# Kernel optimization log

Hardware: AMD Instinct MI355X
Metric: run time of the kernel (lower is better)

The kernel has to match this reference:

```python
import jax, jax.numpy as jnp
import numpy as np

N_NODES = 50000
N_EDGES = 600000
N_GRAPHS = 512
DIM = 128
N_FEAT = 78
N_LAYERS = 4
BN_EPS = 1e-5


def setup_inputs() -> dict:
    key = jax.random.key(0)
    ks = jax.random.split(key, 12)
    w = lambda k, s: (jax.random.normal(k, s, jnp.float32) * 0.05)
    x = jax.random.normal(ks[0], (N_NODES, N_FEAT), jnp.float32)
    edge_index = jax.random.randint(ks[1], (2, N_EDGES), 0, N_NODES)
    batch = jnp.sort(jax.random.randint(ks[2], (N_NODES,), 0, N_GRAPHS))
    return {
        "x": x,
        "edge_index": edge_index,
        "batch": batch,
        "ini_w1": w(ks[3], (N_FEAT, DIM)),
        "ini_b1": jnp.zeros((DIM,), jnp.float32),
        "ini_w2": w(ks[4], (DIM, DIM)),
        "ini_b2": jnp.zeros((DIM,), jnp.float32),
        "gin_w1": w(ks[5], (N_LAYERS, DIM, DIM)),
        "gin_b1": jnp.zeros((N_LAYERS, DIM), jnp.float32),
        "gin_w2": w(ks[6], (N_LAYERS, DIM, DIM)),
        "gin_b2": jnp.zeros((N_LAYERS, DIM), jnp.float32),
        "bn_gamma": jnp.ones((N_LAYERS, DIM), jnp.float32),
        "bn_beta": jnp.zeros((N_LAYERS, DIM), jnp.float32),
        "layer_w": w(ks[7], (N_LAYERS,)),  # Conv2d(L,1,(1,1)) weight
        "layer_b": jnp.zeros((1,), jnp.float32),
    }


def reference(x, edge_index, batch, ini_w1, ini_b1, ini_w2, ini_b2,
              gin_w1, gin_b1, gin_w2, gin_b2, bn_gamma, bn_beta,
              layer_w, layer_b):
    # ini_embed: Linear -> ReLU -> Linear
    h = jnp.maximum(x @ ini_w1 + ini_b1, 0.0) @ ini_w2 + ini_b2  # [N, D]
    src, dst = edge_index[0], edge_index[1]
    embeds = []
    for i in range(N_LAYERS):
        # GINConv (eps=0): mlp(x_i + sum_{j->i} x_j)
        agg = jax.ops.segment_sum(h[src], dst, num_segments=N_NODES)
        z = h + agg
        z = jnp.maximum(z @ gin_w1[i] + gin_b1[i], 0.0) @ gin_w2[i] + gin_b2[i]
        z = jnp.maximum(z, 0.0)  # F.relu after conv
        # BatchNorm1d (training mode: batch stats, biased var)
        mean = jnp.mean(z, axis=0)
        var = jnp.mean((z - mean) ** 2, axis=0)
        h = (z - mean) * jax.lax.rsqrt(var + BN_EPS) * bn_gamma[i] + bn_beta[i]
        embeds.append(h)
    layer_nodes = jnp.stack(embeds, axis=1)  # [N, L, D]
    # layer_conv Conv2d(L,1,(1,1)): learned weighted sum over layer axis + bias
    pos_global_node = jnp.einsum('nld,l->nd', layer_nodes, layer_w) + layer_b
    # global_add_pool over graphs
    pos_global_graph = jax.ops.segment_sum(pos_global_node, batch,
                                           num_segments=N_GRAPHS)  # [G, D]
    return pos_global_graph
```

## Files before the change

kernel.cpp:

```cpp
#include <hip/hip_runtime.h>

#define N_NODES  50000
#define N_EDGES  600000
#define N_GRAPHS 512
#define DIM      128
#define N_FEAT   78
#define N_LAYERS 4
#define BN_EPS   1e-5f
#define SLOT_CAP 64
#define LDA      136
#define NPART    16

#define NBKT     196
#define NBLK_BIN 128
#define BCAP     64
#define EDGES_PER_BIN ((N_EDGES + NBLK_BIN - 1) / NBLK_BIN)

#define GSTART_BLOCKS 196
#define ZERO_BLOCKS 512
#define GBLOCKS ((N_NODES + 63) / 64)
#define TW_ELEMS (10 * 16384)
#define BN_FLOATS (N_LAYERS * NPART * 256)
#define TWB ((TW_ELEMS + BN_FLOATS + 255) / 256)

typedef __attribute__((ext_vector_type(8))) _Float16 f16x8;
typedef __attribute__((ext_vector_type(4))) float f32x4;

static __device__ __forceinline__ short f2h(float f) {
    _Float16 h = (_Float16)f;
    union { _Float16 h; short s; } u; u.h = h;
    return u.s;
}
static __device__ __forceinline__ float h2f(ushort s) {
    union { ushort s; _Float16 h; } u; u.s = s;
    return (float)u.h;
}


__global__ __launch_bounds__(256) void prep(const float* __restrict__ ini_w1,
                                            const float* __restrict__ ini_w2,
                                            const float* __restrict__ gw1,
                                            const float* __restrict__ gw2,
                                            short* __restrict__ wt,
                                            float* __restrict__ bnstat,
                                            const int* __restrict__ src,
                                            const int* __restrict__ dst,
                                            const int* __restrict__ batch,
                                            int* __restrict__ bcnt,
                                            uint* __restrict__ bpool,
                                            int* __restrict__ gstart,
                                            float* __restrict__ gsum,
                                            float* __restrict__ gssq) {
    __shared__ int lcur[NBKT];
    int tid = threadIdx.x;
    int b = blockIdx.x;
    if (b < TWB) {
        int gid = b * 256 + tid;
        if (gid < TW_ELEMS) {
            int m = gid >> 14;
            int idx = gid & 16383;
            int n = idx >> 7;
            int k = idx & 127;
            const float* s;
            int K = 128;
            if (m == 0) { s = ini_w1; K = N_FEAT; }
            else if (m == 1) s = ini_w2;
            else if (m < 6) s = gw1 + (m - 2) * 16384;
            else s = gw2 + (m - 6) * 16384;
            float v = (k < K) ? s[k * 128 + n] : 0.f;
            wt[m * 16384 + n * 128 + k] = f2h(v);
        } else {
            int bi = gid - TW_ELEMS;
            if (bi < BN_FLOATS) bnstat[bi] = 0.0f;
        }
        return;
    }
    b -= TWB;
    if (b < NBLK_BIN) {
        for (int i = tid; i < NBKT; i += 256) lcur[i] = 0;
        __syncthreads();
        int base = b * EDGES_PER_BIN;
        int lim = min(base + EDGES_PER_BIN, N_EDGES);
        for (int e = base + tid; e < lim; e += 256) {
            int d = dst[e];
            int s = src[e];
            int bk = d >> 8;
            int p = atomicAdd(&lcur[bk], 1);
            if (p < BCAP)
                bpool[(bk * NBLK_BIN + b) * BCAP + p] =
                    ((uint)(d & 255) << 16) | (uint)s;
        }
        __syncthreads();
        for (int i = tid; i < NBKT; i += 256) bcnt[b * NBKT + i] = lcur[i];
        return;
    }
    b -= NBLK_BIN;
    if (b < GSTART_BLOCKS) {
        int n = b * 256 + tid;
        if (n < N_NODES) {
            int g = batch[n];
            int gp = (n == 0) ? -1 : batch[n - 1];
            for (int gg = gp + 1; gg <= g; ++gg) gstart[gg] = n;
            if (n == N_NODES - 1)
                for (int gg = g + 1; gg <= N_GRAPHS; ++gg) gstart[gg] = N_NODES;
        }
        return;
    }
    b -= GSTART_BLOCKS;
    float4 z = make_float4(0.f, 0.f, 0.f, 0.f);
    float* bse = (b < 256) ? gsum : gssq;
    int off = (b & 255) * 1024 + tid * 4;
    *(float4*)&bse[off] = z;
}


__global__ __launch_bounds__(256, 4) void ini_fused(const float* __restrict__ x,
                                                    const short* __restrict__ Wt1,
                                                    const float* __restrict__ b1,
                                                    const short* __restrict__ Wt2,
                                                    const float* __restrict__ b2,
                                                    ushort* __restrict__ Cout,
                                                    const uint* __restrict__ bpool,
                                                    const int* __restrict__ bcnt,
                                                    int* __restrict__ cnt,
                                                    ushort* __restrict__ slot) {
    __shared__ short smem[2 * 64 * LDA];
    int tid = threadIdx.x;

    if (blockIdx.x >= GBLOCKS) {
        int bkt = blockIdx.x - GBLOCKS;
        ushort* lslot = (ushort*)smem;
        int* lcnt = (int*)((char*)smem + 32768);
        int* rcnt = (int*)((char*)smem + 33792);
        lcnt[tid] = 0;
        if (tid < NBLK_BIN) rcnt[tid] = min(bcnt[tid * NBKT + bkt], BCAP);
        __syncthreads();
        const uint* pool = bpool + (size_t)bkt * NBLK_BIN * BCAP;
        #pragma unroll 1
        for (int i = tid; i < NBLK_BIN * BCAP; i += 256) {
            int run = i >> 6;
            int pos = i & (BCAP - 1);
            if (pos < rcnt[run]) {
                uint u = pool[i];
                int ls = u >> 16;
                int p = atomicAdd(&lcnt[ls], 1);
                if (p < SLOT_CAP) lslot[ls * SLOT_CAP + p] = (ushort)(u & 0xffffu);
            }
        }
        __syncthreads();
        {
            int n2 = min(lcnt[tid], SLOT_CAP);
            ushort* L = lslot + tid * SLOT_CAP;
            for (int i = 1; i < n2; ++i) {
                ushort key = L[i];
                int j = i - 1;
                while (j >= 0 && L[j] > key) { L[j + 1] = L[j]; --j; }
                L[j + 1] = key;
            }
        }
        __syncthreads();
        int node0 = bkt << 8;
        int gn = node0 + tid;
        if (gn < N_NODES) cnt[gn] = lcnt[tid];
        #pragma unroll
        for (int j = 0; j < 8; ++j) {
            int i = tid + j * 256;
            int r = i >> 3;
            int c = i & 7;
            int g = node0 + r;
            if (g < N_NODES)
                *(uint4*)&slot[g * SLOT_CAP + c * 8] = *(const uint4*)&lslot[r * SLOT_CAP + c * 8];
        }
        return;
    }

    short* As = smem;
    short* Bs = smem + 64 * LDA;
    int row0 = blockIdx.x * 64;
    int wave = tid >> 6;
    int wlane = tid & 63;
    int rw = wave >> 1;
    int cw = wave & 1;
    int lm = wlane & 15;
    int quad = wlane >> 4;
    const int wrow = (cw * 64 + lm) * 128 + quad * 8;

    f16x8 bcur[4], bnxt[4];
    #pragma unroll
    for (int nt = 0; nt < 4; ++nt)
        bcur[nt] = *(const f16x8*)&Wt1[wrow + nt * 2048];

    for (int i = tid; i < 64 * 25; i += 256) {
        int r = i / 25, c = i % 25;
        *(uint*)&As[r * LDA + 78 + c * 2] = 0u;
    }
    if (row0 + 64 <= N_NODES) {
        const float* xb = x + (size_t)row0 * N_FEAT;
        #pragma unroll
        for (int q = 0; q < 5; ++q) {
            int idx = tid + q * 256;
            if (idx < 1248) {
                float4 f4 = ((const float4*)xb)[idx];
                int f0 = idx * 4;
                As[(f0 / 78) * LDA + (f0 % 78)] = f2h(f4.x);
                int f1 = f0 + 1;
                As[(f1 / 78) * LDA + (f1 % 78)] = f2h(f4.y);
                int f2 = f0 + 2;
                As[(f2 / 78) * LDA + (f2 % 78)] = f2h(f4.z);
                int f3 = f0 + 3;
                As[(f3 / 78) * LDA + (f3 % 78)] = f2h(f4.w);
            }
        }
    } else {
        #pragma unroll
        for (int j = 0; j < 32; ++j) {
            int lin = tid + j * 256;
            int r = lin >> 7;
            int k = lin & 127;
            int gr = row0 + r;
            if (k < N_FEAT) {
                float v = 0.f;
                if (gr < N_NODES) v = x[gr * N_FEAT + k];
                As[r * LDA + k] = f2h(v);
            }
        }
    }
    __syncthreads();

    f32x4 acc[2][4];
    #pragma unroll
    for (int mt = 0; mt < 2; ++mt)
        #pragma unroll
        for (int nt = 0; nt < 4; ++nt)
            acc[mt][nt] = (f32x4){0.f, 0.f, 0.f, 0.f};

    #pragma unroll
    for (int ks = 0; ks < 4; ++ks) {
        if (ks < 3) {
            #pragma unroll
            for (int nt = 0; nt < 4; ++nt)
                bnxt[nt] = *(const f16x8*)&Wt1[wrow + nt * 2048 + (ks + 1) * 32];
        }
        int kb = ks * 32 + quad * 8;
        f16x8 a0 = *(const f16x8*)&As[(rw * 32 + lm) * LDA + kb];
        f16x8 a1 = *(const f16x8*)&As[(rw * 32 + 16 + lm) * LDA + kb];
        #pragma unroll
        for (int nt = 0; nt < 4; ++nt) {
            acc[0][nt] = __builtin_amdgcn_mfma_f32_16x16x32_f16(a0, bcur[nt], acc[0][nt], 0, 0, 0);
            acc[1][nt] = __builtin_amdgcn_mfma_f32_16x16x32_f16(a1, bcur[nt], acc[1][nt], 0, 0, 0);
        }
        #pragma unroll
        for (int nt = 0; nt < 4; ++nt) bcur[nt] = bnxt[nt];
    }

    #pragma unroll
    for (int nt = 0; nt < 4; ++nt) {
        int col = cw * 64 + nt * 16 + lm;
        float bv = b1[col];
        #pragma unroll
        for (int mt = 0; mt < 2; ++mt) {
            #pragma unroll
            for (int r = 0; r < 4; ++r) {
                int row = rw * 32 + mt * 16 + quad * 4 + r;
                Bs[row * LDA + col] = (short)f2h(fmaxf(acc[mt][nt][r] + bv, 0.f));
            }
        }
    }
    #pragma unroll
    for (int nt = 0; nt < 4; ++nt)
        bcur[nt] = *(const f16x8*)&Wt2[wrow + nt * 2048];
    __syncthreads();

    #pragma unroll
    for (int mt = 0; mt < 2; ++mt)
        #pragma unroll
        for (int nt = 0; nt < 4; ++nt)
            acc[mt][nt] = (f32x4){0.f, 0.f, 0.f, 0.f};
    #pragma unroll
    for (int ks = 0; ks < 4; ++ks) {
        if (ks < 3) {
            #pragma unroll
            for (int nt = 0; nt < 4; ++nt)
                bnxt[nt] = *(const f16x8*)&Wt2[wrow + nt * 2048 + (ks + 1) * 32];
        }
        int kb = ks * 32 + quad * 8;
        f16x8 a0 = *(const f16x8*)&Bs[(rw * 32 + lm) * LDA + kb];
        f16x8 a1 = *(const f16x8*)&Bs[(rw * 32 + 16 + lm) * LDA + kb];
        #pragma unroll
        for (int nt = 0; nt < 4; ++nt) {
            acc[0][nt] = __builtin_amdgcn_mfma_f32_16x16x32_f16(a0, bcur[nt], acc[0][nt], 0, 0, 0);
            acc[1][nt] = __builtin_amdgcn_mfma_f32_16x16x32_f16(a1, bcur[nt], acc[1][nt], 0, 0, 0);
        }
        #pragma unroll
        for (int nt = 0; nt < 4; ++nt) bcur[nt] = bnxt[nt];
    }

    ushort* Cs = (ushort*)As;
    #pragma unroll
    for (int nt = 0; nt < 4; ++nt) {
        int col = cw * 64 + nt * 16 + lm;
        float bv = b2[col];
        #pragma unroll
        for (int mt = 0; mt < 2; ++mt) {
            #pragma unroll
            for (int r = 0; r < 4; ++r) {
                int row = rw * 32 + mt * 16 + quad * 4 + r;
                Cs[row * LDA + col] = (ushort)f2h(acc[mt][nt][r] + bv);
            }
        }
    }
    __syncthreads();

    #pragma unroll
    for (int j = 0; j < 4; ++j) {
        int lin = tid + j * 256;
        int r = lin >> 4;
        int kc = lin & 15;
        int gr = row0 + r;
        if (gr < N_NODES)
            *(uint4*)&Cout[gr * 128 + kc * 8] = *(const uint4*)&Cs[r * LDA + kc * 8];
    }
}


__global__ __launch_bounds__(256, 4) void gin_fused(const ushort* __restrict__ Z,
                                                    const int* __restrict__ cnt,
                                                    const ushort* __restrict__ slot,
                                                    const float* __restrict__ bnpart,
                                                    const float* __restrict__ gamma,
                                                    const float* __restrict__ beta,
                                                    const short* __restrict__ Wt1,
                                                    const float* __restrict__ b1,
                                                    const short* __restrict__ Wt2,
                                                    const float* __restrict__ b2,
                                                    ushort* __restrict__ C,
                                                    const int* __restrict__ batch,
                                                    float* __restrict__ gsum,
                                                    float* __restrict__ gssq,
                                                    float* __restrict__ bnpart_out) {
    __shared__ short As[64 * LDA];
    __shared__ short Bs[64 * LDA];
    __shared__ float saff[128], taff[128];
    __shared__ float scr[256];
    __shared__ int sb[64];
    int tid = threadIdx.x;
    int row0 = blockIdx.x * 64;

    int wave = tid >> 6;
    int wlane = tid & 63;
    int rw = wave >> 1;
    int cw = wave & 1;
    int lm = wlane & 15;
    int quad = wlane >> 4;
    const int wrow = (cw * 64 + lm) * 128 + quad * 8;

    if (tid < 128) {
        float s = 1.0f, t = 0.0f;
        if (bnpart) {
            float sum = 0.f, ssq = 0.f;
            #pragma unroll
            for (int p = 0; p < NPART; ++p) {
                sum += bnpart[p * 256 + tid];
                ssq += bnpart[p * 256 + 128 + tid];
            }
            const float invN = 1.0f / (float)N_NODES;
            float m = sum * invN;
            float var = ssq * invN - m * m;
            s = gamma[tid] * rsqrtf(var + BN_EPS);
            t = beta[tid] - m * s;
        }
        saff[tid] = s; taff[tid] = t;
    }
    if (tid < 64) {
        int n = row0 + tid;
        sb[tid] = (n < N_NODES) ? batch[n] : -1;
    }
    __syncthreads();

    {
        int lane = tid & 15;
        int nsub = tid >> 4;
        union U { uint4 u; _Float16 h[8]; };
        union I { uint4 u; ushort s[8]; };
        const uint4* z4 = (const uint4*)Z;
        #pragma unroll 1
        for (int pass = 0; pass < 4; ++pass) {
            int r = pass * 16 + nsub;
            int node = row0 + r;
            float v[8];
            float dsc = 1.0f;
            if (node < N_NODES) {
                U zu; zu.u = z4[node * 16 + lane];
                #pragma unroll
                for (int j = 0; j < 8; ++j) v[j] = (float)zu.h[j];
                int dtrue = cnt[node];
                int d = min(dtrue, SLOT_CAP);
                const ushort* sl = slot + node * SLOT_CAP;
                int e = 0;
                for (; e + 8 <= d; e += 8) {
                    I si; si.u = *(const uint4*)&sl[e];
                    U u[8];
                    #pragma unroll
                    for (int q = 0; q < 8; ++q) u[q].u = z4[(int)si.s[q] * 16 + lane];
                    #pragma unroll
                    for (int j = 0; j < 8; ++j) {
                        float a = ((float)u[0].h[j] + (float)u[1].h[j]) +
                                  ((float)u[2].h[j] + (float)u[3].h[j]);
                        float b = ((float)u[4].h[j] + (float)u[5].h[j]) +
                                  ((float)u[6].h[j] + (float)u[7].h[j]);
                        v[j] += a + b;
                    }
                }
                if (e + 4 <= d) {
                    int s0 = sl[e], s1 = sl[e + 1], s2 = sl[e + 2], s3 = sl[e + 3];
                    U u0, u1, u2, u3;
                    u0.u = z4[s0 * 16 + lane];
                    u1.u = z4[s1 * 16 + lane];
                    u2.u = z4[s2 * 16 + lane];
                    u3.u = z4[s3 * 16 + lane];
                    #pragma unroll
                    for (int j = 0; j < 8; ++j)
                        v[j] += ((float)u0.h[j] + (float)u1.h[j]) +
                                ((float)u2.h[j] + (float)u3.h[j]);
                    e += 4;
                }
                for (; e < d; ++e) {
                    U u; u.u = z4[(int)sl[e] * 16 + lane];
                    #pragma unroll
                    for (int j = 0; j < 8; ++j) v[j] += (float)u.h[j];
                }
                dsc = 1.0f + (float)dtrue;
            } else {
                #pragma unroll
                for (int j = 0; j < 8; ++j) v[j] = 0.f;
                dsc = 0.f;
            }
            #pragma unroll
            for (int j = 0; j < 8; ++j) {
                int dd = lane * 8 + j;
                As[r * LDA + dd] = f2h(saff[dd] * v[j] + dsc * taff[dd]);
            }
        }
    }

    f16x8 bcur[4], bnxt[4];
    #pragma unroll
    for (int nt = 0; nt < 4; ++nt)
        bcur[nt] = *(const f16x8*)&Wt1[wrow + nt * 2048];
    __syncthreads();

    f32x4 acc[2][4];
    #pragma unroll
    for (int mt = 0; mt < 2; ++mt)
        #pragma unroll
        for (int nt = 0; nt < 4; ++nt)
            acc[mt][nt] = (f32x4){0.f, 0.f, 0.f, 0.f};
    #pragma unroll
    for (int ks = 0; ks < 4; ++ks) {
        if (ks < 3) {
            #pragma unroll
            for (int nt = 0; nt < 4; ++nt)
                bnxt[nt] = *(const f16x8*)&Wt1[wrow + nt * 2048 + (ks + 1) * 32];
        }
        int kb = ks * 32 + quad * 8;
        f16x8 a0 = *(const f16x8*)&As[(rw * 32 + lm) * LDA + kb];
        f16x8 a1 = *(const f16x8*)&As[(rw * 32 + 16 + lm) * LDA + kb];
        #pragma unroll
        for (int nt = 0; nt < 4; ++nt) {
            acc[0][nt] = __builtin_amdgcn_mfma_f32_16x16x32_f16(a0, bcur[nt], acc[0][nt], 0, 0, 0);
            acc[1][nt] = __builtin_amdgcn_mfma_f32_16x16x32_f16(a1, bcur[nt], acc[1][nt], 0, 0, 0);
        }
        #pragma unroll
        for (int nt = 0; nt < 4; ++nt) bcur[nt] = bnxt[nt];
    }
    #pragma unroll
    for (int nt = 0; nt < 4; ++nt) {
        int col = cw * 64 + nt * 16 + lm;
        float bv = b1[col];
        #pragma unroll
        for (int mt = 0; mt < 2; ++mt) {
            #pragma unroll
            for (int r = 0; r < 4; ++r) {
                int row = rw * 32 + mt * 16 + quad * 4 + r;
                Bs[row * LDA + col] = (short)f2h(fmaxf(acc[mt][nt][r] + bv, 0.f));
            }
        }
    }
    #pragma unroll
    for (int nt = 0; nt < 4; ++nt)
        bcur[nt] = *(const f16x8*)&Wt2[wrow + nt * 2048];
    __syncthreads();

    #pragma unroll
    for (int mt = 0; mt < 2; ++mt)
        #pragma unroll
        for (int nt = 0; nt < 4; ++nt)
            acc[mt][nt] = (f32x4){0.f, 0.f, 0.f, 0.f};
    #pragma unroll
    for (int ks = 0; ks < 4; ++ks) {
        if (ks < 3) {
            #pragma unroll
            for (int nt = 0; nt < 4; ++nt)
                bnxt[nt] = *(const f16x8*)&Wt2[wrow + nt * 2048 + (ks + 1) * 32];
        }
        int kb = ks * 32 + quad * 8;
        f16x8 c0 = *(const f16x8*)&Bs[(rw * 32 + lm) * LDA + kb];
        f16x8 c1 = *(const f16x8*)&Bs[(rw * 32 + 16 + lm) * LDA + kb];
        #pragma unroll
        for (int nt = 0; nt < 4; ++nt) {
            acc[0][nt] = __builtin_amdgcn_mfma_f32_16x16x32_f16(c0, bcur[nt], acc[0][nt], 0, 0, 0);
            acc[1][nt] = __builtin_amdgcn_mfma_f32_16x16x32_f16(c1, bcur[nt], acc[1][nt], 0, 0, 0);
        }
        #pragma unroll
        for (int nt = 0; nt < 4; ++nt) bcur[nt] = bnxt[nt];
    }
    ushort* Cs = (ushort*)As;
    #pragma unroll
    for (int nt = 0; nt < 4; ++nt) {
        int col = cw * 64 + nt * 16 + lm;
        float bv = b2[col];
        #pragma unroll
        for (int mt = 0; mt < 2; ++mt) {
            #pragma unroll
            for (int r = 0; r < 4; ++r) {
                int row = rw * 32 + mt * 16 + quad * 4 + r;
                Cs[row * LDA + col] = (ushort)f2h(fmaxf(acc[mt][nt][r] + bv, 0.f));
            }
        }
    }
    __syncthreads();

    #pragma unroll
    for (int j = 0; j < 4; ++j) {
        int lin = tid + j * 256;
        int r = lin >> 4;
        int kc = lin & 15;
        int gr = row0 + r;
        if (gr < N_NODES)
            *(uint4*)&C[gr * 128 + kc * 8] = *(const uint4*)&Cs[r * LDA + kc * 8];
    }

    {
        int c = tid & 127;
        int rbase = (tid >> 7) * 32;
        int curg = sb[rbase];
        float rs = 0.f, rss = 0.f;
        float ts = 0.f, tss = 0.f;
        for (int r = rbase; r < rbase + 32; ++r) {
            int g = sb[r];
            if (g < 0) break;
            if (g != curg) {
                atomicAdd(&gsum[curg * 128 + c], rs);
                atomicAdd(&gssq[curg * 128 + c], rss);
                rs = 0.f; rss = 0.f; curg = g;
            }
            float v = h2f(Cs[r * LDA + c]);
            rs += v; rss += v * v;
            ts += v; tss += v * v;
        }
        if (curg >= 0) {
            atomicAdd(&gsum[curg * 128 + c], rs);
            atomicAdd(&gssq[curg * 128 + c], rss);
        }
        if (tid >= 128) { scr[c] = ts; scr[128 + c] = tss; }
        __syncthreads();
        if (tid < 128) {
            float* part = bnpart_out + (blockIdx.x & (NPART - 1)) * 256;
            atomicAdd(&part[c], ts + scr[c]);
            atomicAdd(&part[128 + c], tss + scr[128 + c]);
        }
    }
}


__global__ __launch_bounds__(256) void combine(const float* __restrict__ gsum,
                                               const float* __restrict__ bnstat,
                                               const int* __restrict__ gstart,
                                               const float* __restrict__ gamma,
                                               const float* __restrict__ beta,
                                               const float* __restrict__ LW,
                                               const float* __restrict__ LB,
                                               float* __restrict__ out) {
    int gid = blockIdx.x * 256 + threadIdx.x;
    if (gid >= N_GRAPHS * 128) return;
    int g = gid >> 7;
    int d = gid & 127;
    float c = (float)(gstart[g + 1] - gstart[g]);
    float o = c * LB[0];
    const float invN = 1.0f / (float)N_NODES;
    #pragma unroll
    for (int l = 0; l < N_LAYERS; ++l) {
        const float* part = bnstat + l * NPART * 256;
        float sum = 0.f, ssq = 0.f;
        #pragma unroll
        for (int p = 0; p < NPART; ++p) {
            sum += part[p * 256 + d];
            ssq += part[p * 256 + 128 + d];
        }
        float m = sum * invN;
        float var = ssq * invN - m * m;
        float s = gamma[l * 128 + d] * rsqrtf(var + BN_EPS);
        float t = beta[l * 128 + d] - m * s;
        o += LW[l] * (s * gsum[(l * N_GRAPHS + g) * 128 + d] + c * t);
    }
    out[gid] = o;
}


extern "C" void kernel_launch(void* const* d_in, const int* in_sizes, int n_in,
                              void* d_out, int out_size, void* d_ws, size_t ws_size,
                              hipStream_t stream) {
    const float* x      = (const float*)d_in[0];
    const int*   ei     = (const int*)d_in[1];
    const int*   batch  = (const int*)d_in[2];
    const float* ini_w1 = (const float*)d_in[3];
    const float* ini_b1 = (const float*)d_in[4];
    const float* ini_w2 = (const float*)d_in[5];
    const float* ini_b2 = (const float*)d_in[6];
    const float* gw1    = (const float*)d_in[7];
    const float* gb1    = (const float*)d_in[8];
    const float* gw2    = (const float*)d_in[9];
    const float* gb2    = (const float*)d_in[10];
    const float* gamma  = (const float*)d_in[11];
    const float* beta   = (const float*)d_in[12];
    const float* lw     = (const float*)d_in[13];
    const float* lb     = (const float*)d_in[14];
    float* out = (float*)d_out;

    char* p = (char*)d_ws;
    auto carve = [&](size_t bytes) -> char* {
        char* q = p;
        p += (bytes + 255) & ~(size_t)255;
        return q;
    };
    ushort* z0    = (ushort*)carve(sizeof(ushort) * N_NODES * DIM);
    ushort* z1    = (ushort*)carve(sizeof(ushort) * N_NODES * DIM);
    float* bnstat = (float*)carve(sizeof(float) * BN_FLOATS);
    float* gsum   = (float*)carve(sizeof(float) * N_LAYERS * N_GRAPHS * DIM);
    float* gssq   = (float*)carve(sizeof(float) * N_LAYERS * N_GRAPHS * DIM);
    short* wbf    = (short*)carve(sizeof(short) * 10 * 128 * 128);
    int* gstart   = (int*)carve(sizeof(int) * (N_GRAPHS + 1));
    int* cnt      = (int*)carve(sizeof(int) * N_NODES);
    ushort* slot  = (ushort*)carve(sizeof(ushort) * N_NODES * SLOT_CAP);
    int* bcnt     = (int*)carve(sizeof(int) * NBLK_BIN * NBKT);
    uint* bpool   = (uint*)carve(sizeof(uint) * NBKT * NBLK_BIN * BCAP);

    const int* src = ei;
    const int* dst = ei + N_EDGES;

    prep<<<TWB + NBLK_BIN + GSTART_BLOCKS + ZERO_BLOCKS, 256, 0, stream>>>(
        ini_w1, ini_w2, gw1, gw2, wbf, bnstat,
        src, dst, batch, bcnt, bpool, gstart, gsum, gssq);

    ini_fused<<<GBLOCKS + NBKT, 256, 0, stream>>>(
        x, wbf, ini_b1, wbf + 16384, ini_b2, z0,
        bpool, bcnt, cnt, slot);

    ushort* zprev = z0;
    ushort* znext = z1;
    for (int i = 0; i < N_LAYERS; ++i) {
        const float* bp_in = (i == 0) ? nullptr : bnstat + (i - 1) * NPART * 256;
        const float* gptr  = (i == 0) ? gamma : gamma + (i - 1) * DIM;
        const float* bptr  = (i == 0) ? beta : beta + (i - 1) * DIM;
        gin_fused<<<GBLOCKS, 256, 0, stream>>>(
            zprev, cnt, slot, bp_in, gptr, bptr,
            wbf + (2 + i) * 16384, gb1 + i * DIM,
            wbf + (6 + i) * 16384, gb2 + i * DIM, znext, batch,
            gsum + i * N_GRAPHS * DIM, gssq + i * N_GRAPHS * DIM,
            bnstat + i * NPART * 256);
        ushort* tmp = zprev; zprev = znext; znext = tmp;
    }
    combine<<<(N_GRAPHS * 128 + 255) / 256, 256, 0, stream>>>(
        gsum, bnstat, gstart, gamma, beta, lw, lb, out);
}
```

Measured before the change: 339.6 us.

## Drop per-node neighbor sort and simplify input tile load

```diff
diff --git a/kernel.cpp b/kernel.cpp
--- a/kernel.cpp
+++ b/kernel.cpp
@@ -148,17 +148,6 @@
             }
         }
         __syncthreads();
-        {
-            int n2 = min(lcnt[tid], SLOT_CAP);
-            ushort* L = lslot + tid * SLOT_CAP;
-            for (int i = 1; i < n2; ++i) {
-                ushort key = L[i];
-                int j = i - 1;
-                while (j >= 0 && L[j] > key) { L[j + 1] = L[j]; --j; }
-                L[j + 1] = key;
-            }
-        }
-        __syncthreads();
         int node0 = bkt << 8;
         int gn = node0 + tid;
         if (gn < N_NODES) cnt[gn] = lcnt[tid];
@@ -190,40 +179,15 @@
     for (int nt = 0; nt < 4; ++nt)
         bcur[nt] = *(const f16x8*)&Wt1[wrow + nt * 2048];
 
-    for (int i = tid; i < 64 * 25; i += 256) {
-        int r = i / 25, c = i % 25;
-        *(uint*)&As[r * LDA + 78 + c * 2] = 0u;
-    }
-    if (row0 + 64 <= N_NODES) {
-        const float* xb = x + (size_t)row0 * N_FEAT;
-        #pragma unroll
-        for (int q = 0; q < 5; ++q) {
-            int idx = tid + q * 256;
-            if (idx < 1248) {
-                float4 f4 = ((const float4*)xb)[idx];
-                int f0 = idx * 4;
-                As[(f0 / 78) * LDA + (f0 % 78)] = f2h(f4.x);
-                int f1 = f0 + 1;
-                As[(f1 / 78) * LDA + (f1 % 78)] = f2h(f4.y);
-                int f2 = f0 + 2;
-                As[(f2 / 78) * LDA + (f2 % 78)] = f2h(f4.z);
-                int f3 = f0 + 3;
-                As[(f3 / 78) * LDA + (f3 % 78)] = f2h(f4.w);
-            }
-        }
-    } else {
-        #pragma unroll
-        for (int j = 0; j < 32; ++j) {
-            int lin = tid + j * 256;
-            int r = lin >> 7;
-            int k = lin & 127;
-            int gr = row0 + r;
-            if (k < N_FEAT) {
-                float v = 0.f;
-                if (gr < N_NODES) v = x[gr * N_FEAT + k];
-                As[r * LDA + k] = f2h(v);
-            }
-        }
+    #pragma unroll
+    for (int j = 0; j < 32; ++j) {
+        int lin = tid + j * 256;
+        int r = lin >> 7;
+        int k = lin & 127;
+        int gr = row0 + r;
+        float v = 0.f;
+        if (gr < N_NODES && k < N_FEAT) v = x[gr * N_FEAT + k];
+        As[r * LDA + k] = f2h(v);
     }
     __syncthreads();
 
```

Result: faster. 314.6 us (-7.3%).
